# Kernel tuning notes

Hardware: AMD Instinct MI355X
Metric: run time of the kernel (lower is better)

The kernel has to match this reference:

```python
import jax, jax.numpy as jnp
import numpy as np

NUM_NODE = 50000
NUM_REL = 50
NUM_EDGE = 1_000_000
NUM_TRI = 2_000_000
HIDDEN = 64


def setup_inputs() -> dict:
    key = jax.random.key(0)
    ks = jax.random.split(key, 9)
    rel_emb = jax.random.normal(ks[0], (NUM_REL, HIDDEN), dtype=jnp.float32)
    W_msg = jax.random.normal(ks[1], (2 * HIDDEN, HIDDEN), dtype=jnp.float32) / np.sqrt(2 * HIDDEN)
    W_upd = jax.random.normal(ks[2], (2 * HIDDEN, HIDDEN), dtype=jnp.float32) / np.sqrt(2 * HIDDEN)
    src = jax.random.randint(ks[3], (NUM_EDGE,), 0, NUM_NODE, dtype=jnp.int64 if jax.config.jax_enable_x64 else jnp.int32)
    dst = jax.random.randint(ks[4], (NUM_EDGE,), 0, NUM_NODE, dtype=src.dtype)
    rel = jax.random.randint(ks[5], (NUM_EDGE,), 0, NUM_REL, dtype=src.dtype)
    edge_ab = jax.random.randint(ks[6], (NUM_TRI,), 0, NUM_EDGE, dtype=src.dtype)
    edge_bc = jax.random.randint(ks[7], (NUM_TRI,), 0, NUM_EDGE, dtype=src.dtype)
    edge_ac = jax.random.randint(ks[8], (NUM_TRI,), 0, NUM_EDGE, dtype=src.dtype)
    return {
        "rel_emb": rel_emb, "W_msg": W_msg, "W_upd": W_upd,
        "src": src, "dst": dst, "rel": rel,
        "edge_ab": edge_ab, "edge_bc": edge_bc, "edge_ac": edge_ac,
    }


def reference(rel_emb, W_msg, W_upd, src, dst, rel, edge_ab, edge_bc, edge_ac):
    # Per-edge hidden state from relation embedding: [E, D]
    h = rel_emb[rel]
    num_edge = h.shape[0]
    # Triangle message: combine the two body edges of each grounding. [T, 2D]
    pair = jnp.concatenate([h[edge_ab], h[edge_bc]], axis=-1)
    msg = jax.nn.relu(pair @ W_msg)  # [T, D]
    # Scatter-add messages onto the head edge (a,c): irregular, memory-bound.
    agg = jax.ops.segment_sum(msg, edge_ac, num_segments=num_edge)  # [E, D]
    # Edge update.
    out = jax.nn.relu(jnp.concatenate([h, agg], axis=-1) @ W_upd)  # [E, D]
    return out
```

## Files before the change

### kernel.cpp

```cpp
#include <hip/hip_runtime.h>

#define HIDDEN 64
#define NREL 50
#define NPAIR (NREL * NREL)
#define K_INL 6
#define K_SLOTS 30

typedef int   iv4 __attribute__((ext_vector_type(4)));
typedef float fv4 __attribute__((ext_vector_type(4)));

__global__ void precompute_tables(const float* __restrict__ rel_emb,
                                  const float* __restrict__ W_msg,
                                  const float* __restrict__ W_upd,
                                  const int* __restrict__ rel,
                                  unsigned char* __restrict__ rel8,
                                  int conv_n,
                                  float* __restrict__ M2,
                                  float* __restrict__ Hc) {
    const int p = blockIdx.x;
    const int j = threadIdx.x;

    for (int i = p * HIDDEN + j; i < conv_n; i += NPAIR * HIDDEN)
        rel8[i] = (unsigned char)rel[i];

    const int ra = p / NREL, rb = p % NREL;
    __shared__ float msg[HIDDEN];
    const float* ha = rel_emb + ra * HIDDEN;
    const float* hb = rel_emb + rb * HIDDEN;

    float acc = 0.f;
    #pragma unroll 8
    for (int i = 0; i < HIDDEN; ++i) acc += ha[i] * W_msg[i * HIDDEN + j];
    #pragma unroll 8
    for (int i = 0; i < HIDDEN; ++i) acc += hb[i] * W_msg[(HIDDEN + i) * HIDDEN + j];
    msg[j] = fmaxf(acc, 0.f);
    __syncthreads();

    float acc2 = 0.f;
    #pragma unroll 8
    for (int k = 0; k < HIDDEN; ++k) acc2 += msg[k] * W_upd[(HIDDEN + k) * HIDDEN + j];
    M2[p * HIDDEN + j] = acc2;

    if (p < NREL) {
        float acc3 = 0.f;
        #pragma unroll 8
        for (int i = 0; i < HIDDEN; ++i) acc3 += rel_emb[p * HIDDEN + i] * W_upd[i * HIDDEN + j];
        Hc[p * HIDDEN + j] = acc3;
    }
}

__global__ __launch_bounds__(256) void hist_record(
        const unsigned char* __restrict__ rel8,
        const int* __restrict__ edge_ab,
        const int* __restrict__ edge_bc,
        const int* __restrict__ edge_ac,
        unsigned int* __restrict__ recA,
        unsigned short* __restrict__ recB,
        int num_tri) {
    const int n8 = num_tri >> 3;
    int i = blockIdx.x * blockDim.x + threadIdx.x;
    const int stride = gridDim.x * blockDim.x;
    for (; i < n8; i += stride) {
        const iv4 a0 = __builtin_nontemporal_load((const iv4*)edge_ab + 2 * i);
        const iv4 a1 = __builtin_nontemporal_load((const iv4*)edge_ab + 2 * i + 1);
        const iv4 b0 = __builtin_nontemporal_load((const iv4*)edge_bc + 2 * i);
        const iv4 b1 = __builtin_nontemporal_load((const iv4*)edge_bc + 2 * i + 1);
        const iv4 c0 = __builtin_nontemporal_load((const iv4*)edge_ac + 2 * i);
        const iv4 c1 = __builtin_nontemporal_load((const iv4*)edge_ac + 2 * i + 1);
        int p[8], c[8];
        #pragma unroll
        for (int k = 0; k < 4; ++k) {
            p[k]     = (int)rel8[a0[k]] * NREL + (int)rel8[b0[k]];
            p[k + 4] = (int)rel8[a1[k]] * NREL + (int)rel8[b1[k]];
            c[k]     = c0[k];
            c[k + 4] = c1[k];
        }
        unsigned int r[8];
        #pragma unroll
        for (int k = 0; k < 8; ++k)
            r[k] = atomicAdd(recA + ((size_t)c[k] << 2), 1u);
        #pragma unroll
        for (int k = 0; k < 8; ++k) {
            if (r[k] < K_INL)
                ((unsigned short*)(recA + ((size_t)c[k] << 2) + 1))[r[k]] = (unsigned short)p[k];
            else if (r[k] < K_SLOTS)
                recB[(size_t)c[k] * 24 + (r[k] - K_INL)] = (unsigned short)p[k];
        }
    }
    const int rem = num_tri & 7;
    if (rem && blockIdx.x == gridDim.x - 1 && threadIdx.x < rem) {
        const int t = (num_tri & ~7) + threadIdx.x;
        const int p = (int)rel8[edge_ab[t]] * NREL + (int)rel8[edge_bc[t]];
        const size_t c = (size_t)edge_ac[t];
        const unsigned int r = atomicAdd(recA + (c << 2), 1u);
        if (r < K_INL) ((unsigned short*)(recA + (c << 2) + 1))[r] = (unsigned short)p;
        else if (r < K_SLOTS) recB[c * 24 + (r - K_INL)] = (unsigned short)p;
    }
}

__global__ __launch_bounds__(256) void accumulate_record(
        const unsigned char* __restrict__ rel8,
        const unsigned int* __restrict__ recA,
        const unsigned short* __restrict__ recB,
        const float* __restrict__ M2,
        const float* __restrict__ Hc,
        float* __restrict__ out, int num_edge) {
    const int sub = threadIdx.x >> 4;
    const int l   = threadIdx.x & 15;
    const int estride = gridDim.x * 16;
    int e = blockIdx.x * 16 + sub;
    if (e >= num_edge) return;
    iv4 w = __builtin_nontemporal_load((const iv4*)recA + e);
    int re = rel8[e];
    while (true) {
        const int en = e + estride;
        const bool more = en < num_edge;
        iv4 wn = {};
        int rn = 0;
        if (more) {
            wn = __builtin_nontemporal_load((const iv4*)recA + en);
            rn = rel8[en];
        }
        const int dc  = w.x;
        const int deg = dc < K_SLOTS ? dc : K_SLOTS;
        fv4 acc0 = ((const fv4*)(Hc + re * HIDDEN))[l];
        fv4 acc1 = (fv4)0.f;
        const int s0 = w.y & 0xFFFF, s1 = ((unsigned)w.y) >> 16;
        const int s2 = w.z & 0xFFFF, s3 = ((unsigned)w.z) >> 16;
        const int s4 = w.w & 0xFFFF, s5 = ((unsigned)w.w) >> 16;
        if (deg > 0) acc0 += ((const fv4*)M2)[s0 * 16 + l];
        if (deg > 1) acc1 += ((const fv4*)M2)[s1 * 16 + l];
        if (deg > 2) acc0 += ((const fv4*)M2)[s2 * 16 + l];
        if (deg > 3) acc1 += ((const fv4*)M2)[s3 * 16 + l];
        if (deg > 4) acc0 += ((const fv4*)M2)[s4 * 16 + l];
        if (deg > 5) acc1 += ((const fv4*)M2)[s5 * 16 + l];
        if (deg > K_INL) {
            for (int k = K_INL; k < deg; ++k) {
                const int p = recB[(size_t)e * 24 + (k - K_INL)];
                acc0 += ((const fv4*)M2)[p * 16 + l];
            }
        }
        fv4 o = acc0 + acc1;
        o.x = fmaxf(o.x, 0.f);
        o.y = fmaxf(o.y, 0.f);
        o.z = fmaxf(o.z, 0.f);
        o.w = fmaxf(o.w, 0.f);
        __builtin_nontemporal_store(o, (fv4*)out + (size_t)e * 16 + l);
        if (!more) break;
        e = en; w = wn; re = rn;
    }
}

__global__ void scatter_tri(const int* __restrict__ rel,
                            const int* __restrict__ edge_ab,
                            const int* __restrict__ edge_bc,
                            const int* __restrict__ edge_ac,
                            const float* __restrict__ M2,
                            float* __restrict__ out, int num_tri) {
    const int lane   = threadIdx.x & 63;
    const int wave   = (int)((blockIdx.x * blockDim.x + threadIdx.x) >> 6);
    const int nwaves = (int)((gridDim.x * blockDim.x) >> 6);
    for (int t = wave; t < num_tri; t += nwaves) {
        const int p = rel[edge_ab[t]] * NREL + rel[edge_bc[t]];
        const float v = M2[p * HIDDEN + lane];
        unsafeAtomicAdd(&out[(size_t)edge_ac[t] * HIDDEN + lane], v);
    }
}

__global__ void finalize(const int* __restrict__ rel,
                         const float* __restrict__ Hc,
                         float* __restrict__ out, int num_edge) {
    const int total = num_edge * (HIDDEN / 4);
    int i = blockIdx.x * blockDim.x + threadIdx.x;
    const int stride = gridDim.x * blockDim.x;
    for (; i < total; i += stride) {
        const int e = i >> 4;
        const int q = i & 15;
        float4 a = ((const float4*)out)[i];
        float4 h = ((const float4*)(Hc + rel[e] * HIDDEN))[q];
        float4 o;
        o.x = fmaxf(a.x + h.x, 0.f);
        o.y = fmaxf(a.y + h.y, 0.f);
        o.z = fmaxf(a.z + h.z, 0.f);
        o.w = fmaxf(a.w + h.w, 0.f);
        ((float4*)out)[i] = o;
    }
}

extern "C" void kernel_launch(void* const* d_in, const int* in_sizes, int n_in,
                              void* d_out, int out_size, void* d_ws, size_t ws_size,
                              hipStream_t stream) {
    const float* rel_emb = (const float*)d_in[0];
    const float* W_msg   = (const float*)d_in[1];
    const float* W_upd   = (const float*)d_in[2];
    const int* rel     = (const int*)d_in[5];
    const int* edge_ab = (const int*)d_in[6];
    const int* edge_bc = (const int*)d_in[7];
    const int* edge_ac = (const int*)d_in[8];
    float* out = (float*)d_out;

    const int num_edge = in_sizes[5];
    const int num_tri  = in_sizes[6];

    char* ws = (char*)d_ws;
    size_t off = 0;
    auto alloc = [&](size_t bytes) { char* p = ws + off; off = (off + bytes + 255) & ~(size_t)255; return p; };
    float*          M2   = (float*)alloc((size_t)NPAIR * HIDDEN * 4);
    float*          Hc   = (float*)alloc((size_t)NREL * HIDDEN * 4);
    unsigned char*  rel8 = (unsigned char*)alloc((size_t)num_edge);
    unsigned int*   recA = (unsigned int*)alloc((size_t)num_edge * 16);
    unsigned short* recB = (unsigned short*)alloc((size_t)num_edge * 48);
    const size_t required = off;

    const bool fast = (ws_size >= required);

    if (fast) {
        hipMemsetAsync(recA, 0, (size_t)num_edge * 16, stream);
        precompute_tables<<<NPAIR, HIDDEN, 0, stream>>>(rel_emb, W_msg, W_upd,
                                                        rel, rel8, num_edge, M2, Hc);
        const int n8 = num_tri >> 3;
        int hblocks = (n8 + 255) / 256;
        if (hblocks < 1) hblocks = 1;
        hist_record<<<hblocks, 256, 0, stream>>>(rel8, edge_ab, edge_bc, edge_ac,
                                                 recA, recB, num_tri);
        int ablocks = (num_edge + 15) / 16;
        if (ablocks > 16384) ablocks = 16384;
        accumulate_record<<<ablocks, 256, 0, stream>>>(rel8, recA, recB, M2, Hc,
                                                       out, num_edge);
    } else {
        precompute_tables<<<NPAIR, HIDDEN, 0, stream>>>(rel_emb, W_msg, W_upd,
                                                        rel, (unsigned char*)d_ws, 0, M2, Hc);
        hipMemsetAsync(d_out, 0, (size_t)out_size * sizeof(float), stream);
        scatter_tri<<<8192, 256, 0, stream>>>(rel, edge_ab, edge_bc, edge_ac, M2, out, num_tri);
        const int total4 = num_edge * (HIDDEN / 4);
        int fin_blocks = (total4 + 255) / 256;
        if (fin_blocks > 65535 * 8) fin_blocks = 65535 * 8;
        finalize<<<fin_blocks, 256, 0, stream>>>(rel, Hc, out, num_edge);
    }
}
```

Baseline: 473.4 us.

## Privatize per-edge histogram records per XCD with workgroup-scope atomics

The per-edge record array is replicated once per XCD (selected from the hardware XCC_ID register), and the count atomics use workgroup scope so they can resolve in the local L2 instead of going device-wide. Entries beyond two inline slots per XCD go through a shared overflow counter and a smaller overflow buffer. The accumulate kernel reads all eight per-XCD records through lane shuffles. This adds a larger memset, eight times the record footprint, and a second global atomic for overflow entries. Correctness depends on no block migrating across XCDs and on workgroup-scope atomics being coherent within one XCD's L2.

```diff
diff --git a/kernel.cpp b/kernel.cpp
--- a/kernel.cpp
+++ b/kernel.cpp
@@ -3,11 +3,19 @@
 #define HIDDEN 64
 #define NREL 50
 #define NPAIR (NREL * NREL)
-#define K_INL 6
-#define K_SLOTS 30
-
+#define NXCD 8
+#define K_INL 2
+#define K_OVF 16
+
+typedef int   iv2 __attribute__((ext_vector_type(2)));
 typedef int   iv4 __attribute__((ext_vector_type(4)));
 typedef float fv4 __attribute__((ext_vector_type(4)));
+
+__device__ __forceinline__ unsigned int get_xcc() {
+    unsigned int x;
+    asm("s_getreg_b32 %0, hwreg(HW_REG_XCC_ID, 0, 4)" : "=s"(x));
+    return x & 7u;
+}
 
 __global__ void precompute_tables(const float* __restrict__ rel_emb,
                                   const float* __restrict__ W_msg,
@@ -55,8 +63,10 @@
         const int* __restrict__ edge_bc,
         const int* __restrict__ edge_ac,
         unsigned int* __restrict__ recA,
+        unsigned int* __restrict__ ovf,
         unsigned short* __restrict__ recB,
-        int num_tri) {
+        int num_tri, int num_edge) {
+    unsigned int* myA = recA + (size_t)get_xcc() * ((size_t)num_edge * 2);
     const int n8 = num_tri >> 3;
     int i = blockIdx.x * blockDim.x + threadIdx.x;
     const int stride = gridDim.x * blockDim.x;
@@ -78,29 +88,37 @@
         unsigned int r[8];
         #pragma unroll
         for (int k = 0; k < 8; ++k)
-            r[k] = atomicAdd(recA + ((size_t)c[k] << 2), 1u);
+            r[k] = __hip_atomic_fetch_add(myA + (size_t)c[k] * 2, 1u,
+                                          __ATOMIC_RELAXED, __HIP_MEMORY_SCOPE_WORKGROUP);
         #pragma unroll
         for (int k = 0; k < 8; ++k) {
-            if (r[k] < K_INL)
-                ((unsigned short*)(recA + ((size_t)c[k] << 2) + 1))[r[k]] = (unsigned short)p[k];
-            else if (r[k] < K_SLOTS)
-                recB[(size_t)c[k] * 24 + (r[k] - K_INL)] = (unsigned short)p[k];
+            if (r[k] < K_INL) {
+                ((unsigned short*)(myA + (size_t)c[k] * 2 + 1))[r[k]] = (unsigned short)p[k];
+            } else {
+                const unsigned int ro = atomicAdd(&ovf[c[k]], 1u);
+                if (ro < K_OVF) recB[(size_t)c[k] * K_OVF + ro] = (unsigned short)p[k];
+            }
         }
     }
     const int rem = num_tri & 7;
     if (rem && blockIdx.x == gridDim.x - 1 && threadIdx.x < rem) {
         const int t = (num_tri & ~7) + threadIdx.x;
         const int p = (int)rel8[edge_ab[t]] * NREL + (int)rel8[edge_bc[t]];
-        const size_t c = (size_t)edge_ac[t];
-        const unsigned int r = atomicAdd(recA + (c << 2), 1u);
-        if (r < K_INL) ((unsigned short*)(recA + (c << 2) + 1))[r] = (unsigned short)p;
-        else if (r < K_SLOTS) recB[c * 24 + (r - K_INL)] = (unsigned short)p;
+        const size_t cc = (size_t)edge_ac[t];
+        const unsigned int r = __hip_atomic_fetch_add(myA + cc * 2, 1u,
+                                  __ATOMIC_RELAXED, __HIP_MEMORY_SCOPE_WORKGROUP);
+        if (r < K_INL) ((unsigned short*)(myA + cc * 2 + 1))[r] = (unsigned short)p;
+        else {
+            const unsigned int ro = atomicAdd(&ovf[cc], 1u);
+            if (ro < K_OVF) recB[cc * K_OVF + ro] = (unsigned short)p;
+        }
     }
 }
 
 __global__ __launch_bounds__(256) void accumulate_record(
         const unsigned char* __restrict__ rel8,
         const unsigned int* __restrict__ recA,
+        const unsigned int* __restrict__ ovf,
         const unsigned short* __restrict__ recB,
         const float* __restrict__ M2,
         const float* __restrict__ Hc,
@@ -108,37 +126,29 @@
     const int sub = threadIdx.x >> 4;
     const int l   = threadIdx.x & 15;
     const int estride = gridDim.x * 16;
-    int e = blockIdx.x * 16 + sub;
-    if (e >= num_edge) return;
-    iv4 w = __builtin_nontemporal_load((const iv4*)recA + e);
-    int re = rel8[e];
-    while (true) {
-        const int en = e + estride;
-        const bool more = en < num_edge;
-        iv4 wn = {};
-        int rn = 0;
-        if (more) {
-            wn = __builtin_nontemporal_load((const iv4*)recA + en);
-            rn = rel8[en];
-        }
-        const int dc  = w.x;
-        const int deg = dc < K_SLOTS ? dc : K_SLOTS;
+    const size_t cstride = (size_t)num_edge * 2;
+    for (int e = blockIdx.x * 16 + sub; e < num_edge; e += estride) {
+        iv2 w = {0, 0};
+        int ov = 0;
+        if (l < NXCD)
+            w = *(const iv2*)(recA + cstride * (size_t)l + (size_t)e * 2);
+        else if (l == 8)
+            ov = (int)ovf[e];
+        ov = __shfl(ov, 8, 16);
+        const int re = rel8[e];
         fv4 acc0 = ((const fv4*)(Hc + re * HIDDEN))[l];
         fv4 acc1 = (fv4)0.f;
-        const int s0 = w.y & 0xFFFF, s1 = ((unsigned)w.y) >> 16;
-        const int s2 = w.z & 0xFFFF, s3 = ((unsigned)w.z) >> 16;
-        const int s4 = w.w & 0xFFFF, s5 = ((unsigned)w.w) >> 16;
-        if (deg > 0) acc0 += ((const fv4*)M2)[s0 * 16 + l];
-        if (deg > 1) acc1 += ((const fv4*)M2)[s1 * 16 + l];
-        if (deg > 2) acc0 += ((const fv4*)M2)[s2 * 16 + l];
-        if (deg > 3) acc1 += ((const fv4*)M2)[s3 * 16 + l];
-        if (deg > 4) acc0 += ((const fv4*)M2)[s4 * 16 + l];
-        if (deg > 5) acc1 += ((const fv4*)M2)[s5 * 16 + l];
-        if (deg > K_INL) {
-            for (int k = K_INL; k < deg; ++k) {
-                const int p = recB[(size_t)e * 24 + (k - K_INL)];
-                acc0 += ((const fv4*)M2)[p * 16 + l];
-            }
+        #pragma unroll
+        for (int k = 0; k < NXCD; ++k) {
+            const int cnt = __shfl(w.x, k, 16);
+            const int ss  = __shfl(w.y, k, 16);
+            if (cnt > 0) acc0 += ((const fv4*)M2)[(ss & 0xFFFF) * 16 + l];
+            if (cnt > 1) acc1 += ((const fv4*)M2)[(int)(((unsigned)ss) >> 16) * 16 + l];
+        }
+        const int no = ov < K_OVF ? ov : K_OVF;
+        for (int k = 0; k < no; ++k) {
+            const int p = recB[(size_t)e * K_OVF + k];
+            acc0 += ((const fv4*)M2)[p * 16 + l];
         }
         fv4 o = acc0 + acc1;
         o.x = fmaxf(o.x, 0.f);
@@ -146,8 +156,6 @@
         o.z = fmaxf(o.z, 0.f);
         o.w = fmaxf(o.w, 0.f);
         __builtin_nontemporal_store(o, (fv4*)out + (size_t)e * 16 + l);
-        if (!more) break;
-        e = en; w = wn; re = rn;
     }
 }
 
@@ -208,24 +216,26 @@
     float*          M2   = (float*)alloc((size_t)NPAIR * HIDDEN * 4);
     float*          Hc   = (float*)alloc((size_t)NREL * HIDDEN * 4);
     unsigned char*  rel8 = (unsigned char*)alloc((size_t)num_edge);
-    unsigned int*   recA = (unsigned int*)alloc((size_t)num_edge * 16);
-    unsigned short* recB = (unsigned short*)alloc((size_t)num_edge * 48);
+    unsigned int*   recA = (unsigned int*)alloc((size_t)num_edge * 8 * NXCD);
+    unsigned int*   ovf  = (unsigned int*)alloc((size_t)num_edge * 4);
+    unsigned short* recB = (unsigned short*)alloc((size_t)num_edge * K_OVF * 2);
     const size_t required = off;
 
     const bool fast = (ws_size >= required);
 
     if (fast) {
-        hipMemsetAsync(recA, 0, (size_t)num_edge * 16, stream);
+        hipMemsetAsync(recA, 0, (size_t)num_edge * 8 * NXCD, stream);
+        hipMemsetAsync(ovf, 0, (size_t)num_edge * 4, stream);
         precompute_tables<<<NPAIR, HIDDEN, 0, stream>>>(rel_emb, W_msg, W_upd,
                                                         rel, rel8, num_edge, M2, Hc);
         const int n8 = num_tri >> 3;
         int hblocks = (n8 + 255) / 256;
         if (hblocks < 1) hblocks = 1;
         hist_record<<<hblocks, 256, 0, stream>>>(rel8, edge_ab, edge_bc, edge_ac,
-                                                 recA, recB, num_tri);
+                                                 recA, ovf, recB, num_tri, num_edge);
         int ablocks = (num_edge + 15) / 16;
         if (ablocks > 16384) ablocks = 16384;
-        accumulate_record<<<ablocks, 256, 0, stream>>>(rel8, recA, recB, M2, Hc,
+        accumulate_record<<<ablocks, 256, 0, stream>>>(rel8, recA, ovf, recB, M2, Hc,
                                                        out, num_edge);
     } else {
         precompute_tables<<<NPAIR, HIDDEN, 0, stream>>>(rel_emb, W_msg, W_upd,
```

Result: slower. 532.8 us (+12.5%).

## Partition triangles into 64-edge buckets and accumulate per bucket in LDS

Applied to the files above, without the earlier changes.

Replaces the per-edge record slots (fixed inline plus overflow slots) with per-bucket counters and 512-entry buffers holding packed (pair, local edge) keys. The accumulate kernel loads a bucket's keys into shared memory, and each 16-lane group finds its edge's entries via ballot and shuffle. This aims to reduce scattered record memory and atomic spread, at the cost of heavier contention on fewer counters and a linear key scan per edge. It also removes the per-edge 30-triangle truncation, though buckets are still capped at 512.

```diff
diff --git a/kernel.cpp b/kernel.cpp
--- a/kernel.cpp
+++ b/kernel.cpp
@@ -3,8 +3,8 @@
 #define HIDDEN 64
 #define NREL 50
 #define NPAIR (NREL * NREL)
-#define K_INL 6
-#define K_SLOTS 30
+#define BEDGE 64
+#define CAP 512
 
 typedef int   iv4 __attribute__((ext_vector_type(4)));
 typedef float fv4 __attribute__((ext_vector_type(4)));
@@ -49,13 +49,13 @@
     }
 }
 
-__global__ __launch_bounds__(256) void hist_record(
+__global__ __launch_bounds__(256) void partition_tri(
         const unsigned char* __restrict__ rel8,
         const int* __restrict__ edge_ab,
         const int* __restrict__ edge_bc,
         const int* __restrict__ edge_ac,
-        unsigned int* __restrict__ recA,
-        unsigned short* __restrict__ recB,
+        unsigned int* __restrict__ cur,
+        unsigned int* __restrict__ buf,
         int num_tri) {
     const int n8 = num_tri >> 3;
     int i = blockIdx.x * blockDim.x + threadIdx.x;
@@ -78,76 +78,68 @@
         unsigned int r[8];
         #pragma unroll
         for (int k = 0; k < 8; ++k)
-            r[k] = atomicAdd(recA + ((size_t)c[k] << 2), 1u);
+            r[k] = atomicAdd(&cur[c[k] >> 6], 1u);
         #pragma unroll
-        for (int k = 0; k < 8; ++k) {
-            if (r[k] < K_INL)
-                ((unsigned short*)(recA + ((size_t)c[k] << 2) + 1))[r[k]] = (unsigned short)p[k];
-            else if (r[k] < K_SLOTS)
-                recB[(size_t)c[k] * 24 + (r[k] - K_INL)] = (unsigned short)p[k];
-        }
+        for (int k = 0; k < 8; ++k)
+            if (r[k] < CAP)
+                buf[(size_t)(c[k] >> 6) * CAP + r[k]] =
+                    ((unsigned int)p[k] << 6) | ((unsigned int)c[k] & 63u);
     }
     const int rem = num_tri & 7;
     if (rem && blockIdx.x == gridDim.x - 1 && threadIdx.x < rem) {
         const int t = (num_tri & ~7) + threadIdx.x;
         const int p = (int)rel8[edge_ab[t]] * NREL + (int)rel8[edge_bc[t]];
-        const size_t c = (size_t)edge_ac[t];
-        const unsigned int r = atomicAdd(recA + (c << 2), 1u);
-        if (r < K_INL) ((unsigned short*)(recA + (c << 2) + 1))[r] = (unsigned short)p;
-        else if (r < K_SLOTS) recB[c * 24 + (r - K_INL)] = (unsigned short)p;
-    }
-}
-
-__global__ __launch_bounds__(256) void accumulate_record(
+        const int c = edge_ac[t];
+        const unsigned int r = atomicAdd(&cur[c >> 6], 1u);
+        if (r < CAP)
+            buf[(size_t)(c >> 6) * CAP + r] =
+                ((unsigned int)p << 6) | ((unsigned int)c & 63u);
+    }
+}
+
+__global__ __launch_bounds__(256) void accumulate_bucket(
         const unsigned char* __restrict__ rel8,
-        const unsigned int* __restrict__ recA,
-        const unsigned short* __restrict__ recB,
+        const unsigned int* __restrict__ cur,
+        const unsigned int* __restrict__ buf,
         const float* __restrict__ M2,
         const float* __restrict__ Hc,
         float* __restrict__ out, int num_edge) {
-    const int sub = threadIdx.x >> 4;
-    const int l   = threadIdx.x & 15;
-    const int estride = gridDim.x * 16;
-    int e = blockIdx.x * 16 + sub;
-    if (e >= num_edge) return;
-    iv4 w = __builtin_nontemporal_load((const iv4*)recA + e);
-    int re = rel8[e];
-    while (true) {
-        const int en = e + estride;
-        const bool more = en < num_edge;
-        iv4 wn = {};
-        int rn = 0;
-        if (more) {
-            wn = __builtin_nontemporal_load((const iv4*)recA + en);
-            rn = rel8[en];
-        }
-        const int dc  = w.x;
-        const int deg = dc < K_SLOTS ? dc : K_SLOTS;
-        fv4 acc0 = ((const fv4*)(Hc + re * HIDDEN))[l];
-        fv4 acc1 = (fv4)0.f;
-        const int s0 = w.y & 0xFFFF, s1 = ((unsigned)w.y) >> 16;
-        const int s2 = w.z & 0xFFFF, s3 = ((unsigned)w.z) >> 16;
-        const int s4 = w.w & 0xFFFF, s5 = ((unsigned)w.w) >> 16;
-        if (deg > 0) acc0 += ((const fv4*)M2)[s0 * 16 + l];
-        if (deg > 1) acc1 += ((const fv4*)M2)[s1 * 16 + l];
-        if (deg > 2) acc0 += ((const fv4*)M2)[s2 * 16 + l];
-        if (deg > 3) acc1 += ((const fv4*)M2)[s3 * 16 + l];
-        if (deg > 4) acc0 += ((const fv4*)M2)[s4 * 16 + l];
-        if (deg > 5) acc1 += ((const fv4*)M2)[s5 * 16 + l];
-        if (deg > K_INL) {
-            for (int k = K_INL; k < deg; ++k) {
-                const int p = recB[(size_t)e * 24 + (k - K_INL)];
-                acc0 += ((const fv4*)M2)[p * 16 + l];
+    __shared__ unsigned int lk[CAP];
+    const int b = blockIdx.x;
+    const unsigned int craw = cur[b];
+    const int cnt = craw < CAP ? (int)craw : CAP;
+    for (int t = threadIdx.x; t < cnt; t += 256)
+        lk[t] = buf[(size_t)b * CAP + t];
+    __syncthreads();
+
+    const int g     = threadIdx.x >> 4;
+    const int l     = threadIdx.x & 15;
+    const int shift = threadIdx.x & 48;
+
+    for (int le = g; le < BEDGE; le += 16) {
+        const int e = b * BEDGE + le;
+        if (e >= num_edge) continue;
+        const int re = rel8[e];
+        fv4 acc = ((const fv4*)(Hc + re * HIDDEN))[l];
+        for (int base = 0; base < cnt; base += 16) {
+            const int idx = base + l;
+            const unsigned int key = (idx < cnt) ? lk[idx] : 0u;
+            const bool m = (idx < cnt) && ((int)(key & 63u) == le);
+            const unsigned long long bal = __ballot(m);
+            unsigned int mask = (unsigned int)((bal >> shift) & 0xFFFFull);
+            while (mask) {
+                const int bit = __ffs(mask) - 1;
+                mask &= mask - 1;
+                const int p = __shfl((int)(key >> 6), bit, 16);
+                acc += ((const fv4*)M2)[p * 16 + l];
             }
         }
-        fv4 o = acc0 + acc1;
+        fv4 o = acc;
         o.x = fmaxf(o.x, 0.f);
         o.y = fmaxf(o.y, 0.f);
         o.z = fmaxf(o.z, 0.f);
         o.w = fmaxf(o.w, 0.f);
         __builtin_nontemporal_store(o, (fv4*)out + (size_t)e * 16 + l);
-        if (!more) break;
-        e = en; w = wn; re = rn;
     }
 }
 
@@ -201,32 +193,31 @@
 
     const int num_edge = in_sizes[5];
     const int num_tri  = in_sizes[6];
+    const int NB = (num_edge + BEDGE - 1) / BEDGE;
 
     char* ws = (char*)d_ws;
     size_t off = 0;
     auto alloc = [&](size_t bytes) { char* p = ws + off; off = (off + bytes + 255) & ~(size_t)255; return p; };
-    float*          M2   = (float*)alloc((size_t)NPAIR * HIDDEN * 4);
-    float*          Hc   = (float*)alloc((size_t)NREL * HIDDEN * 4);
-    unsigned char*  rel8 = (unsigned char*)alloc((size_t)num_edge);
-    unsigned int*   recA = (unsigned int*)alloc((size_t)num_edge * 16);
-    unsigned short* recB = (unsigned short*)alloc((size_t)num_edge * 48);
+    float*         M2   = (float*)alloc((size_t)NPAIR * HIDDEN * 4);
+    float*         Hc   = (float*)alloc((size_t)NREL * HIDDEN * 4);
+    unsigned char* rel8 = (unsigned char*)alloc((size_t)num_edge);
+    unsigned int*  cur  = (unsigned int*)alloc((size_t)NB * 4);
+    unsigned int*  buf  = (unsigned int*)alloc((size_t)NB * CAP * 4);
     const size_t required = off;
 
     const bool fast = (ws_size >= required);
 
     if (fast) {
-        hipMemsetAsync(recA, 0, (size_t)num_edge * 16, stream);
+        hipMemsetAsync(cur, 0, (size_t)NB * 4, stream);
         precompute_tables<<<NPAIR, HIDDEN, 0, stream>>>(rel_emb, W_msg, W_upd,
                                                         rel, rel8, num_edge, M2, Hc);
         const int n8 = num_tri >> 3;
-        int hblocks = (n8 + 255) / 256;
-        if (hblocks < 1) hblocks = 1;
-        hist_record<<<hblocks, 256, 0, stream>>>(rel8, edge_ab, edge_bc, edge_ac,
-                                                 recA, recB, num_tri);
-        int ablocks = (num_edge + 15) / 16;
-        if (ablocks > 16384) ablocks = 16384;
-        accumulate_record<<<ablocks, 256, 0, stream>>>(rel8, recA, recB, M2, Hc,
-                                                       out, num_edge);
+        int pblocks = (n8 + 255) / 256;
+        if (pblocks < 1) pblocks = 1;
+        partition_tri<<<pblocks, 256, 0, stream>>>(rel8, edge_ab, edge_bc, edge_ac,
+                                                   cur, buf, num_tri);
+        accumulate_bucket<<<NB, 256, 0, stream>>>(rel8, cur, buf, M2, Hc,
+                                                  out, num_edge);
     } else {
         precompute_tables<<<NPAIR, HIDDEN, 0, stream>>>(rel_emb, W_msg, W_upd,
                                                         rel, (unsigned char*)d_ws, 0, M2, Hc);
```

Measured after the change: 465.4 us. Within noise of the previous version (-1.7%).
